# Kernel tuning notes

Measured on AMD Instinct MI355X. Metric: run time of the kernel, lower is better.

## Reference

```python
import jax, jax.numpy as jnp
import numpy as np

D_MODEL = 1024
NUM_HEADS = 16
D_K = D_MODEL // NUM_HEADS
SCALE = D_K ** -0.5
NEG = -1e9


def _split_heads(t):
    B, L, D = t.shape
    return t.reshape(B, L, NUM_HEADS, D_K).transpose(0, 2, 1, 3)  # (B,H,L,dk)


def _tropical_scores(Q, K):
    # max over d_k of Q[...,i,d] + K[...,j,d] without materializing (B,H,L,L,dk)
    Qd = jnp.moveaxis(Q, -1, 0)  # (dk,B,H,L)
    Kd = jnp.moveaxis(K, -1, 0)
    B, H, L, _ = Q.shape
    init = jnp.full((B, H, L, L), -jnp.inf, Q.dtype)
    def step(carry, qk):
        q, k = qk  # (B,H,L) each
        return jnp.maximum(carry, q[..., :, None] + k[..., None, :]), None
    out, _ = jax.lax.scan(step, init, (Qd, Kd))
    return out


def setup_inputs() -> dict:
    key = jax.random.key(0)
    ks = jax.random.split(key, 10)
    B, L = 2, 1024
    x = jax.random.normal(ks[0], (B, L, D_MODEL), dtype=jnp.float32)
    # causal mask (B,1,L,L)
    mask = jnp.broadcast_to(jnp.tril(jnp.ones((L, L), dtype=bool)), (B, 1, L, L))
    s = 0.02
    Wq = jax.random.normal(ks[1], (D_MODEL, D_MODEL), jnp.float32) * s
    Wk = jax.random.normal(ks[2], (D_MODEL, D_MODEL), jnp.float32) * s
    Wv = jax.random.normal(ks[3], (D_MODEL, D_MODEL), jnp.float32) * s
    Wo = jax.random.normal(ks[4], (D_MODEL, D_MODEL), jnp.float32) * s
    bq = jnp.zeros((D_MODEL,), jnp.float32)
    bk = jnp.zeros((D_MODEL,), jnp.float32)
    bv = jnp.zeros((D_MODEL,), jnp.float32)
    bo = jnp.zeros((D_MODEL,), jnp.float32)
    # score_gate: weight zero-init, bias = -2.0 (as in torch module)
    Wg = jnp.zeros((NUM_HEADS, D_MODEL), jnp.float32)
    bg = jnp.full((NUM_HEADS,), -2.0, jnp.float32)
    # log temperatures, init_temp=1.0 -> log(1)=0
    log_temps = jnp.zeros((NUM_HEADS,), jnp.float32)
    return {"x": x, "mask": mask, "Wq": Wq, "bq": bq, "Wk": Wk, "bk": bk,
            "Wv": Wv, "bv": bv, "Wo": Wo, "bo": bo, "Wg": Wg, "bg": bg,
            "log_temps": log_temps}


def reference(x, mask, Wq, bq, Wk, bk, Wv, bv, Wo, bo, Wg, bg, log_temps):
    B, L, D = x.shape
    Q = _split_heads(x @ Wq.T + bq)
    K = _split_heads(x @ Wk.T + bk)
    V = _split_heads(x @ Wv.T + bv)
    class_scores = jnp.einsum('bhqd,bhkd->bhqk', Q, K) * SCALE
    trop_scores = _tropical_scores(Q, K) * SCALE
    # per-query, per-head gate g in (0,1): (B,L,H) -> (B,H,L,1)
    g = jax.nn.sigmoid(x @ Wg.T + bg).transpose(0, 2, 1)[..., None]
    scores = g * trop_scores + (1.0 - g) * class_scores
    scores = jnp.where(mask, scores, NEG)
    tau = jnp.clip(jnp.exp(log_temps), 0.02, 10.0).reshape(1, NUM_HEADS, 1, 1)
    attn = jax.nn.softmax(scores / tau, axis=-1)
    out = jnp.einsum('bhqk,bhkd->bhqd', attn, V)
    out = out.transpose(0, 2, 1, 3).reshape(B, L, D)
    return out @ Wo.T + bo, attn
```

## Files before the change

kernel.cpp:

```cpp
#include <hip/hip_runtime.h>


typedef _Float16 f16;
typedef __attribute__((ext_vector_type(2))) _Float16 h2;
typedef __attribute__((ext_vector_type(8))) _Float16 f16x8;
typedef __attribute__((ext_vector_type(4))) float f32x4;

__device__ inline f32x4 mfma_f16(f16x8 a, f16x8 b, f32x4 c) {
    return __builtin_amdgcn_mfma_f32_16x16x32_f16(a, b, c, 0, 0, 0);
}

__device__ inline void async_copy16(const f16* g, f16* l) {
    __builtin_amdgcn_global_load_lds((const __attribute__((address_space(1))) void*)g,
                                     (__attribute__((address_space(3))) void*)l, 16, 0, 0);
}

__device__ inline float dot2acc(h2 a, h2 b, float c) {
#if __has_builtin(__builtin_amdgcn_fdot2)
    return __builtin_amdgcn_fdot2(a, b, c, false);
#else
    c = fmaf((float)a[0], (float)b[0], c);
    return fmaf((float)a[1], (float)b[1], c);
#endif
}

__global__ __launch_bounds__(256) void cvt_all(const float* __restrict__ x,
                                               const float* __restrict__ Wq,
                                               const float* __restrict__ Wk,
                                               const float* __restrict__ Wv,
                                               const float* __restrict__ Wo,
                                               f16* __restrict__ x16,
                                               f16* __restrict__ w16,
                                               f16* __restrict__ wo16) {
    int i = blockIdx.x * 256 + threadIdx.x;
    const float* s;
    f16* d;
    int off;
    if (i < 524288)       { s = x;  d = x16;             off = i; }
    else if (i < 786432)  { s = Wq; d = w16;             off = i - 524288; }
    else if (i < 1048576) { s = Wk; d = w16 + (1 << 20); off = i - 786432; }
    else if (i < 1310720) { s = Wv; d = w16 + (2 << 20); off = i - 1048576; }
    else                  { s = Wo; d = wo16;            off = i - 1310720; }
    float4 v = *(const float4*)(s + (size_t)off * 4);
    f16 o[4] = {(f16)v.x, (f16)v.y, (f16)v.z, (f16)v.w};
    *(uint2*)(d + (size_t)off * 4) = *(uint2*)o;
}

__global__ __launch_bounds__(256) void gate_kernel(const float* __restrict__ x,
                                                   const float* __restrict__ Wg,
                                                   const float* __restrict__ bg,
                                                   float* __restrict__ gbuf) {
    const int row = blockIdx.x;
    const int t = threadIdx.x;
    const int h = t >> 4, li = t & 15;
    const float* xp = x + (size_t)row * 1024;
    const float* wp = Wg + (size_t)h * 1024;
    float acc = 0.f;
#pragma unroll
    for (int j = 0; j < 16; ++j) {
        int d = li * 4 + j * 64;
        float4 xv = *(const float4*)(xp + d);
        float4 wv = *(const float4*)(wp + d);
        acc = fmaf(xv.x, wv.x, acc);
        acc = fmaf(xv.y, wv.y, acc);
        acc = fmaf(xv.z, wv.z, acc);
        acc = fmaf(xv.w, wv.w, acc);
    }
#pragma unroll
    for (int o = 8; o > 0; o >>= 1) acc += __shfl_xor(acc, o);
    if (li == 0) gbuf[(size_t)row * 16 + h] = 1.0f / (1.0f + __expf(-(acc + bg[h])));
}

template <bool OUT16, bool VTR>
__global__ __launch_bounds__(256) void gemm128(const f16* __restrict__ A,
                                               const f16* __restrict__ B,
                                               void* __restrict__ Cv,
                                               const float* __restrict__ b0,
                                               const float* __restrict__ b1,
                                               const float* __restrict__ b2,
                                               f16* __restrict__ vt,
                                               int K, int lda, int ldb, int ldc) {
    __shared__ f16 At[128 * 32];
    __shared__ f16 Bt[64 * 32];
    const int t = threadIdx.x;
    const int m0 = blockIdx.y * 128, n0 = blockIdx.x * 64;
    const int wave = t >> 6, lane = t & 63;
    const int l16 = lane & 15, quad = lane >> 4;
    const int wm = (wave >> 1) * 64, wn = (wave & 1) * 32;
    const int sr = t >> 2, sc = (t & 3) * 8;
    f32x4 acc[4][2] = {};
    for (int k0 = 0; k0 < K; k0 += 32) {
        __syncthreads();
#pragma unroll
        for (int i = 0; i < 2; ++i)
            async_copy16(A + (size_t)(m0 + sr + i * 64) * lda + k0 + sc, &At[t * 8 + i * 2048]);
        async_copy16(B + (size_t)(n0 + sr) * ldb + k0 + sc, &Bt[t * 8]);
        __syncthreads();
        f16x8 af[4], bfr[2];
#pragma unroll
        for (int i = 0; i < 4; ++i)
            af[i] = *(const f16x8*)&At[(wm + i * 16 + l16) * 32 + quad * 8];
#pragma unroll
        for (int i = 0; i < 2; ++i)
            bfr[i] = *(const f16x8*)&Bt[(wn + i * 16 + l16) * 32 + quad * 8];
#pragma unroll
        for (int mi = 0; mi < 4; ++mi)
#pragma unroll
            for (int ni = 0; ni < 2; ++ni)
                acc[mi][ni] = mfma_f16(af[mi], bfr[ni], acc[mi][ni]);
    }
#pragma unroll
    for (int mi = 0; mi < 4; ++mi) {
#pragma unroll
        for (int ni = 0; ni < 2; ++ni) {
            int gcol = n0 + wn + ni * 16 + l16;
            const float* bp = (gcol < 1024) ? b0 : (gcol < 2048 ? b1 : b2);
            float bias = bp[gcol & 1023];
            if (VTR && n0 >= 2048) {
                int hd = gcol - 2048;
                int h = hd >> 6, d = hd & 63;
                int k0r = m0 + wm + mi * 16 + quad * 4;
                int b = k0r >> 10;
                f16 o4[4];
#pragma unroll
                for (int rg = 0; rg < 4; ++rg) o4[rg] = (f16)(acc[mi][ni][rg] + bias);
                *(uint2*)&vt[((size_t)((b * 16 + h) * 64 + d)) * 1024 + (k0r & 1023)] =
                    *(uint2*)o4;
            } else {
#pragma unroll
                for (int rg = 0; rg < 4; ++rg) {
                    int grow = m0 + wm + mi * 16 + quad * 4 + rg;
                    float v = acc[mi][ni][rg] + bias;
                    if (OUT16)
                        ((f16*)Cv)[(size_t)grow * ldc + gcol] = (f16)v;
                    else
                        ((float*)Cv)[(size_t)grow * ldc + gcol] = v;
                }
            }
        }
    }
}

__global__ __launch_bounds__(256) void scores_fused(const f16* __restrict__ qkv16,
                                                    const f16* __restrict__ vt16,
                                                    const float* __restrict__ gbuf,
                                                    const float* __restrict__ log_temps,
                                                    float* __restrict__ attn,
                                                    f16* __restrict__ oh) {
    __shared__ f16 Qs[16][64];
    __shared__ f16 Ssm[16][1032];
    __shared__ float gsm[16];
    const int t = threadIdx.x;
    const int qt = 63 - (blockIdx.x >> 5);
    const int bh = blockIdx.x & 31;
    const int b = bh & 1, h = bh >> 1;
    const int q0 = qt << 4;
    {
        int rr = t >> 4, cc = (t & 15) * 4;
        *(uint2*)&Qs[rr][cc] =
            *(const uint2*)(qkv16 + (size_t)(b * 1024 + q0 + rr) * 3072 + h * 64 + cc);
    }
    if (t < 16) gsm[t] = gbuf[(size_t)(b * 1024 + q0 + t) * 16 + h];
    float tau = __expf(log_temps[h]);
    tau = fminf(fmaxf(tau, 0.02f), 10.0f);
    const float invtau = 1.0f / tau;
    __syncthreads();

    const int qmax = q0 + 15;
    const int npass = (qmax >> 9) + 1;
    for (int p = 0; p < npass; ++p) {
        const int k1 = (p << 9) + t;
        const int k2 = k1 + 256;
        const bool a1 = (k1 <= qmax), a2 = (k2 <= qmax);
        if (a1) {
            const f16* Kp1 = qkv16 + (size_t)(b * 1024 + k1) * 3072 + 1024 + h * 64;
            h2 kr1[32], kr2[32];
#pragma unroll
            for (int i = 0; i < 8; ++i) *(f16x8*)&kr1[i * 4] = ((const f16x8*)Kp1)[i];
            if (a2) {
                const f16* Kp2 = qkv16 + (size_t)(b * 1024 + k2) * 3072 + 1024 + h * 64;
#pragma unroll
                for (int i = 0; i < 8; ++i) *(f16x8*)&kr2[i * 4] = ((const f16x8*)Kp2)[i];
            }
#pragma unroll 2
            for (int q = 0; q < 16; ++q) {
                h2 qr[32];
#pragma unroll
                for (int i = 0; i < 8; ++i) *(f16x8*)&qr[i * 4] = *(const f16x8*)&Qs[q][i * 8];
                float g = gsm[q];
                {
                    float dot = 0.f;
                    h2 tm2 = {(f16)-65504.f, (f16)-65504.f};
#pragma unroll
                    for (int i = 0; i < 32; ++i) {
                        h2 qa = qr[i];
                        h2 s2 = qa + kr1[i];
                        tm2 = __builtin_elementwise_max(tm2, s2);
                        dot = dot2acc(qa, kr1[i], dot);
                    }
                    float tm = fmaxf((float)tm2[0], (float)tm2[1]);
                    Ssm[q][k1] = (f16)((g * tm + (1.0f - g) * dot) * 0.125f);
                }
                if (a2) {
                    float dot = 0.f;
                    h2 tm2 = {(f16)-65504.f, (f16)-65504.f};
#pragma unroll
                    for (int i = 0; i < 32; ++i) {
                        h2 qa = qr[i];
                        h2 s2 = qa + kr2[i];
                        tm2 = __builtin_elementwise_max(tm2, s2);
                        dot = dot2acc(qa, kr2[i], dot);
                    }
                    float tm = fmaxf((float)tm2[0], (float)tm2[1]);
                    Ssm[q][k2] = (f16)((g * tm + (1.0f - g) * dot) * 0.125f);
                }
            }
        }
    }
    __syncthreads();

    const int lane = t & 63, w = t >> 6;
    const int l16 = lane & 15, quad = lane >> 4;
#pragma unroll
    for (int j = 0; j < 4; ++j) {
        int q = w * 4 + j;
        int qg = q0 + q;
        float m = -1e30f;
        for (int k = lane; k <= qg; k += 64) m = fmaxf(m, (float)Ssm[q][k]);
#pragma unroll
        for (int o = 32; o > 0; o >>= 1) m = fmaxf(m, __shfl_xor(m, o));
        float ssum = 0.f;
        for (int k = lane; k <= qg; k += 64) {
            float e = __expf(((float)Ssm[q][k] - m) * invtau);
            Ssm[q][k] = (f16)e;
            ssum += e;
        }
#pragma unroll
        for (int o = 32; o > 0; o >>= 1) ssum += __shfl_xor(ssum, o);
        float inv = 1.0f / ssum;
        float* orow = attn + ((size_t)((b * 16 + h) * 1024 + qg) << 10);
        for (int k = lane; k < 1024; k += 64) {
            float val = (k <= qg) ? (float)Ssm[q][k] * inv : 0.0f;
            orow[k] = val;
            Ssm[q][k] = (f16)val;
        }
    }
    __syncthreads();

    {
        const int dw = w * 16;
        f32x4 acc = {};
        const int nkt = (q0 + 47) >> 5;
        const f16* Vb = vt16 + ((size_t)((b * 16 + h) * 64 + dw + l16)) * 1024 + quad * 8;
#pragma unroll 4
        for (int kt = 0; kt < nkt; ++kt) {
            const int kb = kt << 5;
            f16x8 a = *(const f16x8*)&Ssm[l16][kb + quad * 8];
            f16x8 bf = *(const f16x8*)(Vb + kb);
            acc = mfma_f16(a, bf, acc);
        }
#pragma unroll
        for (int rg = 0; rg < 4; ++rg)
            oh[(size_t)(b * 1024 + q0 + quad * 4 + rg) * 1024 + h * 64 + dw + l16] =
                (f16)acc[rg];
    }
}

extern "C" void kernel_launch(void* const* d_in, const int* in_sizes, int n_in,
                              void* d_out, int out_size, void* d_ws, size_t ws_size,
                              hipStream_t stream) {
    const float* x  = (const float*)d_in[0];
    const float* Wq = (const float*)d_in[2];
    const float* bq = (const float*)d_in[3];
    const float* Wk = (const float*)d_in[4];
    const float* bk = (const float*)d_in[5];
    const float* Wv = (const float*)d_in[6];
    const float* bv = (const float*)d_in[7];
    const float* Wo = (const float*)d_in[8];
    const float* bo = (const float*)d_in[9];
    const float* Wg = (const float*)d_in[10];
    const float* bg = (const float*)d_in[11];
    const float* lt = (const float*)d_in[12];
    float* out = (float*)d_out;
    float* attn = out + (size_t)2 * 1024 * 1024;

    char* ws = (char*)d_ws;
    const size_t MB = (size_t)1 << 20;
    f16*   x16   = (f16*)ws;
    f16*   w16   = (f16*)(ws + 4 * MB);
    f16*   wo16  = (f16*)(ws + 10 * MB);
    f16*   qkv16 = (f16*)(ws + 12 * MB);
    f16*   vt16  = (f16*)(ws + 24 * MB);
    float* gbuf  = (float*)(ws + 28 * MB);
    f16*   oh16  = (f16*)(ws + 29 * MB);

    cvt_all<<<6144, 256, 0, stream>>>(x, Wq, Wk, Wv, Wo, x16, w16, wo16);
    gate_kernel<<<2048, 256, 0, stream>>>(x, Wg, bg, gbuf);
    gemm128<true, true><<<dim3(48, 16), 256, 0, stream>>>(x16, w16, qkv16, bq, bk, bv,
                                                          vt16, 1024, 1024, 1024, 3072);
    scores_fused<<<2048, 256, 0, stream>>>(qkv16, vt16, gbuf, lt, attn, oh16);
    gemm128<false, false><<<dim3(16, 16), 256, 0, stream>>>(oh16, wo16, out, bo, bo, bo,
                                                            nullptr, 1024, 1024, 1024, 1024);
}
```

Baseline: 304.4 us.

## Compute classic scores with MFMA, fuse gate into scores kernel, restructure tropical loop

The classic Q·K dot product now comes from MFMA tiles written into shared memory, so the scalar loop only does the tropical max-plus reduction, using two independent accumulators and double-buffered K loads with threads mapped per query. The gate sigmoid is computed inside the scores kernel, which drops a separate launch and its buffer. The softmax keeps exponentials in registers instead of writing them back to shared memory and reading them again. In exchange, each block reloads x and Wg to recompute the gate for its rows, the same rows once per head, and the kernel uses more registers.

Measured after the change: 339.7 us. 1.12x slower.

```diff
diff --git a/kernel.cpp b/kernel.cpp
--- a/kernel.cpp
+++ b/kernel.cpp
@@ -13,15 +13,6 @@
 __device__ inline void async_copy16(const f16* g, f16* l) {
     __builtin_amdgcn_global_load_lds((const __attribute__((address_space(1))) void*)g,
                                      (__attribute__((address_space(3))) void*)l, 16, 0, 0);
-}
-
-__device__ inline float dot2acc(h2 a, h2 b, float c) {
-#if __has_builtin(__builtin_amdgcn_fdot2)
-    return __builtin_amdgcn_fdot2(a, b, c, false);
-#else
-    c = fmaf((float)a[0], (float)b[0], c);
-    return fmaf((float)a[1], (float)b[1], c);
-#endif
 }
 
 __global__ __launch_bounds__(256) void cvt_all(const float* __restrict__ x,
@@ -46,31 +37,6 @@
     *(uint2*)(d + (size_t)off * 4) = *(uint2*)o;
 }
 
-__global__ __launch_bounds__(256) void gate_kernel(const float* __restrict__ x,
-                                                   const float* __restrict__ Wg,
-                                                   const float* __restrict__ bg,
-                                                   float* __restrict__ gbuf) {
-    const int row = blockIdx.x;
-    const int t = threadIdx.x;
-    const int h = t >> 4, li = t & 15;
-    const float* xp = x + (size_t)row * 1024;
-    const float* wp = Wg + (size_t)h * 1024;
-    float acc = 0.f;
-#pragma unroll
-    for (int j = 0; j < 16; ++j) {
-        int d = li * 4 + j * 64;
-        float4 xv = *(const float4*)(xp + d);
-        float4 wv = *(const float4*)(wp + d);
-        acc = fmaf(xv.x, wv.x, acc);
-        acc = fmaf(xv.y, wv.y, acc);
-        acc = fmaf(xv.z, wv.z, acc);
-        acc = fmaf(xv.w, wv.w, acc);
-    }
-#pragma unroll
-    for (int o = 8; o > 0; o >>= 1) acc += __shfl_xor(acc, o);
-    if (li == 0) gbuf[(size_t)row * 16 + h] = 1.0f / (1.0f + __expf(-(acc + bg[h])));
-}
-
 template <bool OUT16, bool VTR>
 __global__ __launch_bounds__(256) void gemm128(const f16* __restrict__ A,
                                                const f16* __restrict__ B,
@@ -143,11 +109,13 @@
 
 __global__ __launch_bounds__(256) void scores_fused(const f16* __restrict__ qkv16,
                                                     const f16* __restrict__ vt16,
-                                                    const float* __restrict__ gbuf,
+                                                    const float* __restrict__ x,
+                                                    const float* __restrict__ Wg,
+                                                    const float* __restrict__ bgv,
                                                     const float* __restrict__ log_temps,
                                                     float* __restrict__ attn,
                                                     f16* __restrict__ oh) {
-    __shared__ f16 Qs[16][64];
+    __shared__ f16 Qs[16][80];
     __shared__ f16 Ssm[16][1032];
     __shared__ float gsm[16];
     const int t = threadIdx.x;
@@ -155,72 +123,100 @@
     const int bh = blockIdx.x & 31;
     const int b = bh & 1, h = bh >> 1;
     const int q0 = qt << 4;
+    const int lane = t & 63, w = t >> 6;
+    const int l16 = lane & 15, quad = lane >> 4;
+    const int qmax = q0 + 15;
+
     {
         int rr = t >> 4, cc = (t & 15) * 4;
         *(uint2*)&Qs[rr][cc] =
             *(const uint2*)(qkv16 + (size_t)(b * 1024 + q0 + rr) * 3072 + h * 64 + cc);
     }
-    if (t < 16) gsm[t] = gbuf[(size_t)(b * 1024 + q0 + t) * 16 + h];
+    {
+        int row = t >> 4, ch = t & 15;
+        const float* xp = x + (size_t)(b * 1024 + q0 + row) * 1024 + ch * 64;
+        const float* wp = Wg + (size_t)h * 1024 + ch * 64;
+        float acc = 0.f;
+#pragma unroll
+        for (int j = 0; j < 16; ++j) {
+            float4 xv = *(const float4*)(xp + j * 4);
+            float4 wv = *(const float4*)(wp + j * 4);
+            acc = fmaf(xv.x, wv.x, acc);
+            acc = fmaf(xv.y, wv.y, acc);
+            acc = fmaf(xv.z, wv.z, acc);
+            acc = fmaf(xv.w, wv.w, acc);
+        }
+#pragma unroll
+        for (int o = 8; o > 0; o >>= 1) acc += __shfl_xor(acc, o);
+        if (ch == 0) gsm[row] = 1.0f / (1.0f + __expf(-(acc + bgv[h])));
+    }
     float tau = __expf(log_temps[h]);
     tau = fminf(fmaxf(tau, 0.02f), 10.0f);
     const float invtau = 1.0f / tau;
     __syncthreads();
 
-    const int qmax = q0 + 15;
-    const int npass = (qmax >> 9) + 1;
-    for (int p = 0; p < npass; ++p) {
-        const int k1 = (p << 9) + t;
-        const int k2 = k1 + 256;
-        const bool a1 = (k1 <= qmax), a2 = (k2 <= qmax);
-        if (a1) {
-            const f16* Kp1 = qkv16 + (size_t)(b * 1024 + k1) * 3072 + 1024 + h * 64;
-            h2 kr1[32], kr2[32];
-#pragma unroll
-            for (int i = 0; i < 8; ++i) *(f16x8*)&kr1[i * 4] = ((const f16x8*)Kp1)[i];
-            if (a2) {
-                const f16* Kp2 = qkv16 + (size_t)(b * 1024 + k2) * 3072 + 1024 + h * 64;
-#pragma unroll
-                for (int i = 0; i < 8; ++i) *(f16x8*)&kr2[i * 4] = ((const f16x8*)Kp2)[i];
+    {
+        f16x8 qf0 = *(const f16x8*)&Qs[l16][quad * 8];
+        f16x8 qf1 = *(const f16x8*)&Qs[l16][32 + quad * 8];
+        const f16* Kb = qkv16 + (size_t)(b * 1024 + l16) * 3072 + 1024 + h * 64 + quad * 8;
+        for (int kb = w * 16; kb <= qmax; kb += 64) {
+            f16x8 kf0 = *(const f16x8*)(Kb + (size_t)kb * 3072);
+            f16x8 kf1 = *(const f16x8*)(Kb + (size_t)kb * 3072 + 32);
+            f32x4 acc = {};
+            acc = mfma_f16(kf0, qf0, acc);
+            acc = mfma_f16(kf1, qf1, acc);
+            f16 o4[4];
+#pragma unroll
+            for (int rg = 0; rg < 4; ++rg) o4[rg] = (f16)acc[rg];
+            *(uint2*)&Ssm[l16][kb + quad * 4] = *(uint2*)o4;
+        }
+    }
+    __syncthreads();
+
+    {
+        const int q = t & 15, kg = t >> 4;
+        h2 qr[32];
+#pragma unroll
+        for (int i = 0; i < 8; ++i) *(f16x8*)&qr[i * 4] = *(const f16x8*)&Qs[q][i * 8];
+        const float g = gsm[q];
+        const f16* Kp = qkv16 + (size_t)(b * 1024) * 3072 + 1024 + h * 64;
+        h2 krA[32], krB[32];
+        const int nit = qt + 1;
+
+#define KLOAD(KR, row)                                                        \
+    {                                                                         \
+        const f16* kp_ = Kp + (size_t)(row) * 3072;                           \
+        _Pragma("unroll") for (int i_ = 0; i_ < 8; ++i_)                      \
+            *(f16x8*)&KR[i_ * 4] = ((const f16x8*)kp_)[i_];                   \
+    }
+#define TROP(KR, kk)                                                          \
+    {                                                                         \
+        float dot = (float)Ssm[q][kk];                                        \
+        h2 ta = qr[0] + KR[0], tb = qr[1] + KR[1];                            \
+        _Pragma("unroll") for (int i_ = 2; i_ < 32; i_ += 2) {                \
+            ta = __builtin_elementwise_max(ta, qr[i_] + KR[i_]);              \
+            tb = __builtin_elementwise_max(tb, qr[i_ + 1] + KR[i_ + 1]);      \
+        }                                                                     \
+        h2 tc = __builtin_elementwise_max(ta, tb);                            \
+        float tm = fmaxf((float)tc[0], (float)tc[1]);                         \
+        Ssm[q][kk] = (f16)((g * tm + (1.0f - g) * dot) * 0.125f);             \
+    }
+
+        KLOAD(krA, kg);
+        for (int it = 0; it < nit; it += 2) {
+            int k = it * 16 + kg;
+            if (it + 1 < nit) KLOAD(krB, k + 16);
+            TROP(krA, k);
+            if (it + 1 < nit) {
+                if (it + 2 < nit) KLOAD(krA, k + 32);
+                TROP(krB, k + 16);
             }
-#pragma unroll 2
-            for (int q = 0; q < 16; ++q) {
-                h2 qr[32];
-#pragma unroll
-                for (int i = 0; i < 8; ++i) *(f16x8*)&qr[i * 4] = *(const f16x8*)&Qs[q][i * 8];
-                float g = gsm[q];
-                {
-                    float dot = 0.f;
-                    h2 tm2 = {(f16)-65504.f, (f16)-65504.f};
-#pragma unroll
-                    for (int i = 0; i < 32; ++i) {
-                        h2 qa = qr[i];
-                        h2 s2 = qa + kr1[i];
-                        tm2 = __builtin_elementwise_max(tm2, s2);
-                        dot = dot2acc(qa, kr1[i], dot);
-                    }
-                    float tm = fmaxf((float)tm2[0], (float)tm2[1]);
-                    Ssm[q][k1] = (f16)((g * tm + (1.0f - g) * dot) * 0.125f);
-                }
-                if (a2) {
-                    float dot = 0.f;
-                    h2 tm2 = {(f16)-65504.f, (f16)-65504.f};
-#pragma unroll
-                    for (int i = 0; i < 32; ++i) {
-                        h2 qa = qr[i];
-                        h2 s2 = qa + kr2[i];
-                        tm2 = __builtin_elementwise_max(tm2, s2);
-                        dot = dot2acc(qa, kr2[i], dot);
-                    }
-                    float tm = fmaxf((float)tm2[0], (float)tm2[1]);
-                    Ssm[q][k2] = (f16)((g * tm + (1.0f - g) * dot) * 0.125f);
-                }
-            }
-        }
+        }
+#undef KLOAD
+#undef TROP
     }
     __syncthreads();
 
-    const int lane = t & 63, w = t >> 6;
-    const int l16 = lane & 15, quad = lane >> 4;
 #pragma unroll
     for (int j = 0; j < 4; ++j) {
         int q = w * 4 + j;
@@ -229,18 +225,26 @@
         for (int k = lane; k <= qg; k += 64) m = fmaxf(m, (float)Ssm[q][k]);
 #pragma unroll
         for (int o = 32; o > 0; o >>= 1) m = fmaxf(m, __shfl_xor(m, o));
+        float e[16];
         float ssum = 0.f;
-        for (int k = lane; k <= qg; k += 64) {
-            float e = __expf(((float)Ssm[q][k] - m) * invtau);
-            Ssm[q][k] = (f16)e;
-            ssum += e;
+#pragma unroll
+        for (int i = 0; i < 16; ++i) {
+            int k = lane + i * 64;
+            if (k <= qg) {
+                float v = __expf(((float)Ssm[q][k] - m) * invtau);
+                e[i] = v;
+                ssum += v;
+            } else
+                e[i] = 0.f;
         }
 #pragma unroll
         for (int o = 32; o > 0; o >>= 1) ssum += __shfl_xor(ssum, o);
         float inv = 1.0f / ssum;
         float* orow = attn + ((size_t)((b * 16 + h) * 1024 + qg) << 10);
-        for (int k = lane; k < 1024; k += 64) {
-            float val = (k <= qg) ? (float)Ssm[q][k] * inv : 0.0f;
+#pragma unroll
+        for (int i = 0; i < 16; ++i) {
+            int k = lane + i * 64;
+            float val = e[i] * inv;
             orow[k] = val;
             Ssm[q][k] = (f16)val;
         }
@@ -291,14 +295,12 @@
     f16*   wo16  = (f16*)(ws + 10 * MB);
     f16*   qkv16 = (f16*)(ws + 12 * MB);
     f16*   vt16  = (f16*)(ws + 24 * MB);
-    float* gbuf  = (float*)(ws + 28 * MB);
     f16*   oh16  = (f16*)(ws + 29 * MB);
 
     cvt_all<<<6144, 256, 0, stream>>>(x, Wq, Wk, Wv, Wo, x16, w16, wo16);
-    gate_kernel<<<2048, 256, 0, stream>>>(x, Wg, bg, gbuf);
     gemm128<true, true><<<dim3(48, 16), 256, 0, stream>>>(x16, w16, qkv16, bq, bk, bv,
                                                           vt16, 1024, 1024, 1024, 3072);
-    scores_fused<<<2048, 256, 0, stream>>>(qkv16, vt16, gbuf, lt, attn, oh16);
+    scores_fused<<<2048, 256, 0, stream>>>(qkv16, vt16, x, Wg, bg, lt, attn, oh16);
     gemm128<false, false><<<dim3(16, 16), 256, 0, stream>>>(oh16, wo16, out, bo, bo, bo,
                                                             nullptr, 1024, 1024, 1024, 1024);
 }
```
